# Performance work log

Measured on AMD Instinct MI355X. Metric: run time of the kernel, lower is better.

The kernel has to match this reference:

```python
import jax, jax.numpy as jnp
import numpy as np

N, E, D, G = 50000, 640000, 128, 64
STEPS = 4

def _leaky(z):
    return jnp.where(z >= 0, z, 0.01 * z)

def _lin(x, W, b):
    return x @ W.T + b

def setup_inputs() -> dict:
    key = jax.random.key(0)
    ks = jax.random.split(key, 16)
    s = 0.05
    inp = {
        "x": jax.random.normal(ks[0], (N, D), jnp.float32),
        "x_global": jax.random.normal(ks[1], (G, D), jnp.float32),
        "edge_attr": jax.random.normal(ks[2], (E, 2), jnp.float32),
        # per-step stacked parameters (torch Linear layout [out,in])
        "Wm": jax.random.normal(ks[3], (STEPS, D, D), jnp.float32) * s,
        "bm": jnp.zeros((STEPS, D), jnp.float32),
        "Wa": jax.random.normal(ks[4], (STEPS, D, 2 * D), jnp.float32) * s,
        "ba": jnp.zeros((STEPS, D), jnp.float32),
        "Wgate": jax.random.normal(ks[5], (STEPS, 1, D), jnp.float32) * s,
        "bgate": jnp.zeros((STEPS, 1), jnp.float32),
        "Wfeat": jax.random.normal(ks[6], (STEPS, D, D), jnp.float32) * s,
        "bfeat": jnp.zeros((STEPS, D), jnp.float32),
        "Wt": jax.random.normal(ks[7], (STEPS, D, 2 * D), jnp.float32) * s,
        "bt": jnp.zeros((STEPS, D), jnp.float32),
        "edge_index": jax.random.randint(ks[8], (2, E), 0, N, jnp.int32),
        "batch_ind": jnp.sort(jax.random.randint(ks[9], (N,), 0, G, jnp.int32)),
        "num_graphs": G,
    }
    return inp

def reference(x, x_global, edge_attr, Wm, bm, Wa, ba, Wgate, bgate, Wfeat, bfeat, Wt, bt, edge_index, batch_ind, num_graphs):
    src, dst = edge_index[0], edge_index[1]
    n = x.shape[0]
    for i in range(Wm.shape[0]):
        # GraphNet: gather -> Linear+LeakyReLU -> scatter-max -> concat -> Linear+LeakyReLU + residual
        msg = _leaky(_lin(x[src], Wm[i], bm[i]))                     # [E, agg]
        agg = jax.ops.segment_max(msg, dst, num_segments=n)
        agg = jnp.where(jnp.isfinite(agg), agg, 0.0)                 # PyG fills empty with 0
        x = _leaky(_lin(jnp.concatenate([x, agg], axis=1), Wa[i], ba[i])) + x
        # GlobalNode: attentional aggregation (segment softmax) + transform + residual
        gate = _lin(x, Wgate[i], bgate[i])[:, 0]                     # [N]
        feat = _leaky(_lin(x, Wfeat[i], bfeat[i]))                   # [N, D]
        gmax = jax.ops.segment_max(gate, batch_ind, num_segments=num_graphs)
        gmax = jnp.where(jnp.isfinite(gmax), gmax, 0.0)
        e = jnp.exp(gate - gmax[batch_ind])
        denom = jax.ops.segment_sum(e, batch_ind, num_segments=num_graphs)
        denom = jnp.where(denom == 0, 1.0, denom)
        alpha = e / denom[batch_ind]
        xg = jax.ops.segment_sum(alpha[:, None] * feat, batch_ind, num_segments=num_graphs)
        cat = jnp.concatenate([xg, x_global], axis=1)
        x_global = _leaky(_lin(cat, Wt[i], bt[i])) + x_global
    return (x, x_global)
```

## Files before the change

kernel.cpp:

```cpp
#include <hip/hip_runtime.h>
#include <hip/hip_bf16.h>

#define NN 50000
#define EE 640000
#define DD 128
#define GG 64
#define STEPS 4
#define XP 64
#define NB 196

static inline int cdiv(int a, int b) { return (a + b - 1) / b; }

typedef __attribute__((ext_vector_type(8))) short bf16x8;
typedef __attribute__((ext_vector_type(4))) float f32x4;

__device__ __forceinline__ float lk(float z) { return z >= 0.f ? z : 0.01f * z; }
__device__ __forceinline__ float b2f(short b) { return __uint_as_float(((unsigned)(unsigned short)b) << 16); }
__device__ __forceinline__ float b2fu(unsigned short b) { return __uint_as_float(((unsigned)b) << 16); }
__device__ __forceinline__ unsigned short f2b(float f) {
    unsigned u = __float_as_uint(f);
    return (unsigned short)((u + 0x7FFFu + ((u >> 16) & 1u)) >> 16);
}

__global__ void k_f2b(const float* __restrict__ in, unsigned short* __restrict__ out, int n4) {
    int i = blockIdx.x * blockDim.x + threadIdx.x;
    if (i < n4) {
        float4 v = reinterpret_cast<const float4*>(in)[i];
        ushort4 o;
        o.x = f2b(v.x); o.y = f2b(v.y); o.z = f2b(v.z); o.w = f2b(v.w);
        reinterpret_cast<ushort4*>(out)[i] = o;
    }
}

#define WC1 (STEPS * DD * DD / 4)
#define WC2 (STEPS * DD * 2 * DD / 4)
#define WC3 (STEPS * DD * DD / 4)
__global__ void k_wcvt(const float* __restrict__ Wm, const float* __restrict__ Wa, const float* __restrict__ Wf,
                       unsigned short* __restrict__ Wm_b, unsigned short* __restrict__ Wa_b,
                       unsigned short* __restrict__ Wf_b) {
    int i = blockIdx.x * blockDim.x + threadIdx.x;
    const float* src; unsigned short* dst; int j = i;
    if (j < WC1) { src = Wm; dst = Wm_b; }
    else {
        j -= WC1;
        if (j < WC2) { src = Wa; dst = Wa_b; }
        else {
            j -= WC2;
            if (j >= WC3) return;
            src = Wf; dst = Wf_b;
        }
    }
    float4 v = reinterpret_cast<const float4*>(src)[j];
    ushort4 o;
    o.x = f2b(v.x); o.y = f2b(v.y); o.z = f2b(v.z); o.w = f2b(v.w);
    reinterpret_cast<ushort4*>(dst)[j] = o;
}

__global__ void k_count(const int* __restrict__ dst, int* __restrict__ deg) {
    int e = blockIdx.x * blockDim.x + threadIdx.x;
    if (e < EE) atomicAdd(&deg[dst[e]], 1);
}

__global__ __launch_bounds__(256) void k_scan1(const int* __restrict__ deg, int* __restrict__ off,
                                               int* __restrict__ bsum) {
    __shared__ int ws[4];
    int tid = threadIdx.x, lane = tid & 63, wv = tid >> 6;
    int i = blockIdx.x * 256 + tid;
    int v = (i < NN) ? deg[i] : 0;
    int x = v;
    #pragma unroll
    for (int o = 1; o < 64; o <<= 1) { int t = __shfl_up(x, o); if (lane >= o) x += t; }
    if (lane == 63) ws[wv] = x;
    __syncthreads();
    int wbase = 0;
    #pragma unroll
    for (int p = 0; p < 3; ++p) if (p < wv) wbase += ws[p];
    if (i < NN) off[i] = wbase + x - v;
    if (tid == 255) bsum[blockIdx.x] = wbase + x;
}

__global__ __launch_bounds__(256) void k_scan2(const int* __restrict__ bsum, int* __restrict__ boff,
                                               int* __restrict__ off) {
    __shared__ int ws[4];
    int tid = threadIdx.x, lane = tid & 63, wv = tid >> 6;
    int v = (tid < NB) ? bsum[tid] : 0;
    int x = v;
    #pragma unroll
    for (int o = 1; o < 64; o <<= 1) { int t = __shfl_up(x, o); if (lane >= o) x += t; }
    if (lane == 63) ws[wv] = x;
    __syncthreads();
    int wbase = 0;
    #pragma unroll
    for (int p = 0; p < 3; ++p) if (p < wv) wbase += ws[p];
    if (tid < NB) boff[tid] = wbase + x - v;
    if (tid == 255) off[NN] = wbase + x;
}

__global__ __launch_bounds__(256) void k_scan3(const int* __restrict__ boff, int* __restrict__ off,
                                               int* __restrict__ cursor) {
    int i = blockIdx.x * 256 + threadIdx.x;
    if (i < NN) {
        int o = off[i] + boff[blockIdx.x];
        off[i] = o;
        cursor[i] = o;
    }
}

__global__ void k_fill(const int* __restrict__ src, const int* __restrict__ dst,
                       int* __restrict__ cursor, int* __restrict__ csr) {
    int e = blockIdx.x * blockDim.x + threadIdx.x;
    if (e < EE) {
        int d = dst[e];
        int p = atomicAdd(&cursor[d], 1);
        csr[p] = src[e];
    }
}

__global__ void k_goff(const int* __restrict__ batch, int* __restrict__ goff) {
    int i = blockIdx.x * blockDim.x + threadIdx.x;
    if (i >= NN) return;
    int b = batch[i];
    int prev = (i == 0) ? -1 : batch[i - 1];
    for (int g = prev + 1; g <= b; ++g) goff[g] = i;
    if (i == NN - 1) for (int g = b + 1; g <= GG; ++g) goff[g] = NN;
}

__global__ __launch_bounds__(256) void k_g128(
    const unsigned short* __restrict__ Xb, const unsigned short* __restrict__ W1,
    const float* __restrict__ b1, unsigned short* __restrict__ Yb1)
{
    __shared__ float sY[32 * 128];
    const int tid = threadIdx.x;
    const int wv = tid >> 6, lane = tid & 63;
    const int lo = lane & 15, hi = lane >> 4;
    const int rw = wv >> 1, cw = wv & 1;
    const int n0 = blockIdx.x * 32;
    const int arow = n0 + rw * 16 + lo;
    const bool rvalid = arow < NN;

    bf16x8 a[4];
    #pragma unroll
    for (int kc = 0; kc < 4; ++kc) {
        const int k = kc * 32 + hi * 8;
        a[kc] = rvalid ? *reinterpret_cast<const bf16x8*>(&Xb[(size_t)arow * 128 + k]) : (bf16x8)(short)0;
    }
    f32x4 acc[4];
    #pragma unroll
    for (int t = 0; t < 4; ++t) acc[t] = (f32x4){0.f,0.f,0.f,0.f};
    #pragma unroll
    for (int kc = 0; kc < 4; ++kc) {
        const int k = kc * 32 + hi * 8;
        #pragma unroll
        for (int t = 0; t < 4; ++t) {
            const int o = cw * 64 + t * 16 + lo;
            bf16x8 bv = *reinterpret_cast<const bf16x8*>(&W1[(size_t)o * 128 + k]);
            acc[t] = __builtin_amdgcn_mfma_f32_16x16x32_bf16(a[kc], bv, acc[t], 0, 0, 0);
        }
    }
    const int lrow = rw * 16 + hi * 4;
    const int swz = (hi & 1) << 4;
    #pragma unroll
    for (int t = 0; t < 4; ++t) {
        const int oc = cw * 64 + t * 16 + lo;
        const int col = oc ^ swz;
        const float bc = b1[oc];
        #pragma unroll
        for (int r = 0; r < 4; ++r) sY[(lrow + r) * 128 + col] = lk(acc[t][r] + bc);
    }
    __syncthreads();
    #pragma unroll
    for (int it = 0; it < 2; ++it) {
        const int idx = it * 256 + tid;
        const int row = idx >> 4, ub = (idx & 15) * 8;
        const int n = n0 + row;
        if (n < NN) {
            const int ubx = ub ^ (((row >> 2) & 1) << 4);
            bf16x8 ob;
            #pragma unroll
            for (int j = 0; j < 8; ++j) ob[j] = (short)f2b(sY[row * 128 + ubx + j]);
            *reinterpret_cast<bf16x8*>(&Yb1[(size_t)n * 128 + ub]) = ob;
        }
    }
}

template<bool MSG, bool LAST>
__global__ __launch_bounds__(256) void k_mega(
    const unsigned short* __restrict__ Xb, const unsigned short* __restrict__ Ab,
    const unsigned short* __restrict__ Wa, const float* __restrict__ ba,
    const float* __restrict__ wgf, const float* __restrict__ bgp,
    const unsigned short* __restrict__ Wf, const float* __restrict__ bfp,
    const unsigned short* __restrict__ Wm2, const float* __restrict__ bm2,
    float* __restrict__ Yf, unsigned short* __restrict__ Xbout,
    float* __restrict__ efac, unsigned short* __restrict__ featb,
    unsigned short* __restrict__ ybm)
{
    __shared__ float sY[32 * 128];
    __shared__ unsigned short sXn[32 * 136];
    const int tid = threadIdx.x;
    const int wv = tid >> 6, lane = tid & 63;
    const int lo = lane & 15, hi = lane >> 4;
    const int rw = wv >> 1, cw = wv & 1;
    const int n0 = blockIdx.x * 32;
    const int arow = n0 + rw * 16 + lo;
    const bool rvalid = arow < NN;

    bf16x8 a[8];
    #pragma unroll
    for (int kc = 0; kc < 8; ++kc) {
        const int k = kc * 32 + hi * 8;
        if (rvalid) {
            const unsigned short* base = (kc < 4) ? &Xb[(size_t)arow * 128 + k]
                                                  : &Ab[(size_t)arow * 128 + (k - 128)];
            a[kc] = *reinterpret_cast<const bf16x8*>(base);
        } else a[kc] = (bf16x8)(short)0;
    }

    f32x4 acc1[4];
    #pragma unroll
    for (int t = 0; t < 4; ++t) acc1[t] = (f32x4){0.f,0.f,0.f,0.f};
    #pragma unroll
    for (int kc = 0; kc < 8; ++kc) {
        const int k = kc * 32 + hi * 8;
        #pragma unroll
        for (int t = 0; t < 4; ++t) {
            const int o = cw * 64 + t * 16 + lo;
            bf16x8 bv = *reinterpret_cast<const bf16x8*>(&Wa[(size_t)o * 256 + k]);
            acc1[t] = __builtin_amdgcn_mfma_f32_16x16x32_bf16(a[kc], bv, acc1[t], 0, 0, 0);
        }
    }

    const int lrow = rw * 16 + hi * 4;
    const int swz = (hi & 1) << 4;
    #pragma unroll
    for (int t = 0; t < 4; ++t) {
        const int oc = cw * 64 + t * 16 + lo;
        const int col = oc ^ swz;
        const float bc = ba[oc];
        #pragma unroll
        for (int r = 0; r < 4; ++r) sY[(lrow + r) * 128 + col] = lk(acc1[t][r] + bc);
    }
    __syncthreads();

    {
        const float bg0 = bgp[0];
        #pragma unroll
        for (int it = 0; it < 4; ++it) {
            const int idx = it * 256 + tid;
            const int row = idx >> 5, u4 = (idx & 31) * 4;
            const int n = n0 + row;
            const bool valid = n < NN;
            const int ux = u4 ^ (((row >> 2) & 1) << 4);
            float4 v = *reinterpret_cast<const float4*>(&sY[row * 128 + ux]);
            if (valid) {
                ushort4 rb = *reinterpret_cast<const ushort4*>(&Xb[(size_t)n * 128 + u4]);
                v.x += b2fu(rb.x); v.y += b2fu(rb.y); v.z += b2fu(rb.z); v.w += b2fu(rb.w);
            }
            ushort4 ob;
            ob.x = f2b(v.x); ob.y = f2b(v.y); ob.z = f2b(v.z); ob.w = f2b(v.w);
            if (valid) {
                if (LAST) *reinterpret_cast<float4*>(&Yf[(size_t)n * 128 + u4]) = v;
                else      *reinterpret_cast<ushort4*>(&Xbout[(size_t)n * 128 + u4]) = ob;
            }
            *reinterpret_cast<ushort4*>(&sXn[row * 136 + u4]) = ob;
            float4 wg4 = *reinterpret_cast<const float4*>(&wgf[u4]);
            float gs = valid ? (v.x * wg4.x + v.y * wg4.y + v.z * wg4.z + v.w * wg4.w) : 0.f;
            #pragma unroll
            for (int sh = 16; sh > 0; sh >>= 1) gs += __shfl_xor(gs, sh);
            if ((lane & 31) == 0 && valid) efac[n] = __expf(gs + bg0);
        }
    }
    __syncthreads();

    bf16x8 a2[4];
    #pragma unroll
    for (int kc = 0; kc < 4; ++kc) {
        const int k = kc * 32 + hi * 8;
        a2[kc] = *reinterpret_cast<const bf16x8*>(&sXn[(rw * 16 + lo) * 136 + k]);
    }
    f32x4 accF[4], accM[4];
    #pragma unroll
    for (int t = 0; t < 4; ++t) { accF[t] = (f32x4){0.f,0.f,0.f,0.f}; accM[t] = (f32x4){0.f,0.f,0.f,0.f}; }
    #pragma unroll
    for (int kc = 0; kc < 4; ++kc) {
        const int k = kc * 32 + hi * 8;
        #pragma unroll
        for (int t = 0; t < 4; ++t) {
            const int o = cw * 64 + t * 16 + lo;
            bf16x8 bv = *reinterpret_cast<const bf16x8*>(&Wf[(size_t)o * 128 + k]);
            accF[t] = __builtin_amdgcn_mfma_f32_16x16x32_bf16(a2[kc], bv, accF[t], 0, 0, 0);
            if (MSG) {
                bf16x8 bv2 = *reinterpret_cast<const bf16x8*>(&Wm2[(size_t)o * 128 + k]);
                accM[t] = __builtin_amdgcn_mfma_f32_16x16x32_bf16(a2[kc], bv2, accM[t], 0, 0, 0);
            }
        }
    }
    __syncthreads();

    #pragma unroll
    for (int t = 0; t < 4; ++t) {
        const int oc = cw * 64 + t * 16 + lo;
        const int col = oc ^ swz;
        const float bc = bfp[oc];
        #pragma unroll
        for (int r = 0; r < 4; ++r) sY[(lrow + r) * 128 + col] = lk(accF[t][r] + bc);
    }
    __syncthreads();
    #pragma unroll
    for (int it = 0; it < 2; ++it) {
        const int idx = it * 256 + tid;
        const int row = idx >> 4, ub = (idx & 15) * 8;
        const int n = n0 + row;
        if (n < NN) {
            const int ubx = ub ^ (((row >> 2) & 1) << 4);
            bf16x8 ob;
            #pragma unroll
            for (int j = 0; j < 8; ++j) ob[j] = (short)f2b(sY[row * 128 + ubx + j]);
            *reinterpret_cast<bf16x8*>(&featb[(size_t)n * 128 + ub]) = ob;
        }
    }

    if (MSG) {
        __syncthreads();
        #pragma unroll
        for (int t = 0; t < 4; ++t) {
            const int oc = cw * 64 + t * 16 + lo;
            const int col = oc ^ swz;
            const float bc = bm2[oc];
            #pragma unroll
            for (int r = 0; r < 4; ++r) sY[(lrow + r) * 128 + col] = lk(accM[t][r] + bc);
        }
        __syncthreads();
        #pragma unroll
        for (int it = 0; it < 2; ++it) {
            const int idx = it * 256 + tid;
            const int row = idx >> 4, ub = (idx & 15) * 8;
            const int n = n0 + row;
            if (n < NN) {
                const int ubx = ub ^ (((row >> 2) & 1) << 4);
                bf16x8 ob;
                #pragma unroll
                for (int j = 0; j < 8; ++j) ob[j] = (short)f2b(sY[row * 128 + ubx + j]);
                *reinterpret_cast<bf16x8*>(&ybm[(size_t)n * 128 + ub]) = ob;
            }
        }
    }
}

__global__ __launch_bounds__(256) void k_aggmax(const unsigned short* __restrict__ yb,
                                                const int* __restrict__ off,
                                                const int* __restrict__ csr,
                                                unsigned short* __restrict__ aggb) {
    int gtid = blockIdx.x * blockDim.x + threadIdx.x;
    int node = gtid >> 6;
    if (node >= NN) return;
    int lane = threadIdx.x & 63;
    int slot = lane >> 4, c8 = (lane & 15) * 8;
    int b = off[node], e = off[node + 1];
    int deg = e - b;
    float m[8];
    #pragma unroll
    for (int j = 0; j < 8; ++j) m[j] = -3.4e38f;
    if (deg > 0) {
        int T = (deg + 7) >> 3;
        for (int it = 0; it < T; ++it) {
            int p0 = b + it * 8 + slot;
            int p1 = p0 + 4;
            int i0 = csr[p0 < e ? p0 : b];
            int i1 = csr[p1 < e ? p1 : b];
            bf16x8 v0 = *reinterpret_cast<const bf16x8*>(&yb[(size_t)i0 * 128 + c8]);
            bf16x8 v1 = *reinterpret_cast<const bf16x8*>(&yb[(size_t)i1 * 128 + c8]);
            #pragma unroll
            for (int j = 0; j < 8; ++j) m[j] = fmaxf(m[j], fmaxf(b2f(v0[j]), b2f(v1[j])));
        }
    }
    #pragma unroll
    for (int j = 0; j < 8; ++j) m[j] = fmaxf(m[j], __shfl_xor(m[j], 16));
    #pragma unroll
    for (int j = 0; j < 8; ++j) m[j] = fmaxf(m[j], __shfl_xor(m[j], 32));
    if (slot == 0) {
        bf16x8 o;
        #pragma unroll
        for (int j = 0; j < 8; ++j) o[j] = (deg > 0) ? (short)f2b(m[j]) : (short)0;
        *reinterpret_cast<bf16x8*>(&aggb[(size_t)node * 128 + c8]) = o;
    }
}

__global__ __launch_bounds__(128) void k_xgpart(const float* __restrict__ efac,
                                                const unsigned short* __restrict__ featb,
                                                const int* __restrict__ goff,
                                                float* __restrict__ part, float* __restrict__ parte) {
    int g = blockIdx.x >> 6, p = blockIdx.x & 63;
    int d = threadIdx.x;
    int b = goff[g], e = goff[g + 1];
    int len = e - b;
    int chunk = (len + XP - 1) / XP;
    int s0 = b + p * chunk;
    int s1 = min(e, s0 + chunk);
    float acc = 0.f, acce = 0.f;
    #pragma unroll 4
    for (int i = s0; i < s1; ++i) {
        float ev = efac[i];
        acce += ev;
        acc += ev * b2f(featb[(size_t)i * 128 + d]);
    }
    part[((size_t)g * XP + p) * 128 + d] = acc;
    if (d == 0) parte[(size_t)g * XP + p] = acce;
}

__global__ __launch_bounds__(128) void k_gtrans(const float* __restrict__ part, const float* __restrict__ parte,
                                                const float* __restrict__ Wt, const float* __restrict__ bt,
                                                float* __restrict__ xglob) {
    __shared__ float cat[256];
    int g = blockIdx.x;
    int o = threadIdx.x;
    float xgv = 0.f, se = 0.f;
    #pragma unroll
    for (int p = 0; p < XP; ++p) {
        xgv += part[((size_t)g * XP + p) * 128 + o];
        se  += parte[(size_t)g * XP + p];
    }
    if (se == 0.f) se = 1.f;
    cat[o] = xgv / se;
    cat[128 + o] = xglob[(size_t)g * 128 + o];
    __syncthreads();
    float accv = bt[o];
    const float4* w4 = reinterpret_cast<const float4*>(&Wt[(size_t)o * 256]);
    #pragma unroll 8
    for (int k4 = 0; k4 < 64; ++k4) {
        float4 wv = w4[k4];
        accv += cat[4 * k4 + 0] * wv.x + cat[4 * k4 + 1] * wv.y + cat[4 * k4 + 2] * wv.z + cat[4 * k4 + 3] * wv.w;
    }
    float outv = lk(accv) + cat[128 + o];
    xglob[(size_t)g * 128 + o] = outv;
}

extern "C" void kernel_launch(void* const* d_in, const int* in_sizes, int n_in,
                              void* d_out, int out_size, void* d_ws, size_t ws_size,
                              hipStream_t stream) {
    const float* x_in  = (const float*)d_in[0];
    const float* xg_in = (const float*)d_in[1];
    const float* Wm = (const float*)d_in[3];
    const float* bm = (const float*)d_in[4];
    const float* Wa = (const float*)d_in[5];
    const float* ba = (const float*)d_in[6];
    const float* Wg = (const float*)d_in[7];
    const float* bg = (const float*)d_in[8];
    const float* Wf = (const float*)d_in[9];
    const float* bf = (const float*)d_in[10];
    const float* Wt = (const float*)d_in[11];
    const float* bt = (const float*)d_in[12];
    const int* eidx  = (const int*)d_in[13];
    const int* batch = (const int*)d_in[14];

    float* xout  = (float*)d_out;
    float* xglob = xout + (size_t)NN * DD;

    char* w = (char*)d_ws;
    unsigned short* yb    = (unsigned short*)w; w += (size_t)NN * DD * 2;
    unsigned short* featb = (unsigned short*)w; w += (size_t)NN * DD * 2;
    unsigned short* aggb  = (unsigned short*)w; w += (size_t)NN * DD * 2;
    unsigned short* xb    = (unsigned short*)w; w += (size_t)NN * DD * 2;
    unsigned short* Wm_b  = (unsigned short*)w; w += (size_t)STEPS * DD * DD * 2;
    unsigned short* Wa_b  = (unsigned short*)w; w += (size_t)STEPS * DD * 2 * DD * 2;
    unsigned short* Wf_b  = (unsigned short*)w; w += (size_t)STEPS * DD * DD * 2;
    float* efac   = (float*)w; w += (size_t)NN * 4;
    float* part   = (float*)w; w += (size_t)GG * XP * DD * 4;
    float* parte  = (float*)w; w += (size_t)GG * XP * 4;
    int* deg    = (int*)w; w += (size_t)(NN + 1) * 4;
    int* off    = (int*)w; w += (size_t)(NN + 1) * 4;
    int* cursor = (int*)w; w += (size_t)NN * 4;
    int* csr    = (int*)w; w += (size_t)EE * 4;
    int* goff   = (int*)w; w += (size_t)(GG + 1) * 4;
    int* bsum   = (int*)w; w += (size_t)NB * 4;
    int* boff   = (int*)w; w += (size_t)NB * 4;

    const int* srcI = eidx;
    const int* dstI = eidx + EE;

    hipMemcpyAsync(xglob, xg_in, (size_t)GG * DD * 4, hipMemcpyDeviceToDevice, stream);

    k_f2b<<<cdiv(NN * DD / 4, 256), 256, 0, stream>>>(x_in, xb, NN * DD / 4);
    k_wcvt<<<cdiv(WC1 + WC2 + WC3, 256), 256, 0, stream>>>(Wm, Wa, Wf, Wm_b, Wa_b, Wf_b);

    hipMemsetAsync(deg, 0, (size_t)NN * 4, stream);
    k_count<<<cdiv(EE, 256), 256, 0, stream>>>(dstI, deg);
    k_scan1<<<NB, 256, 0, stream>>>(deg, off, bsum);
    k_scan2<<<1, 256, 0, stream>>>(bsum, boff, off);
    k_scan3<<<NB, 256, 0, stream>>>(boff, off, cursor);
    k_fill<<<cdiv(EE, 256), 256, 0, stream>>>(srcI, dstI, cursor, csr);
    k_goff<<<cdiv(NN, 256), 256, 0, stream>>>(batch, goff);

    const int gemmGrid = cdiv(NN, 32);
    const int aggGrid  = cdiv(NN * 64, 256);

    k_g128<<<gemmGrid, 256, 0, stream>>>(xb, Wm_b, bm, yb);

    for (int i = 0; i < STEPS; ++i) {
        const float* bai = ba + (size_t)i * DD;
        const unsigned short* Wai = Wa_b + (size_t)i * DD * 2 * DD;
        const float* Wgi = Wg + (size_t)i * DD;
        const float* bgi = bg + (size_t)i;
        const unsigned short* Wfi = Wf_b + (size_t)i * DD * DD;
        const float* bfi = bf + (size_t)i * DD;
        const float* Wti = Wt + (size_t)i * DD * 2 * DD;
        const float* bti = bt + (size_t)i * DD;

        k_aggmax<<<aggGrid, 256, 0, stream>>>(yb, off, csr, aggb);
        if (i < STEPS - 1) {
            const unsigned short* Wmn = Wm_b + (size_t)(i + 1) * DD * DD;
            const float* bmn = bm + (size_t)(i + 1) * DD;
            k_mega<true, false><<<gemmGrid, 256, 0, stream>>>(
                xb, aggb, Wai, bai, Wgi, bgi, Wfi, bfi, Wmn, bmn,
                nullptr, xb, efac, featb, yb);
        } else {
            k_mega<false, true><<<gemmGrid, 256, 0, stream>>>(
                xb, aggb, Wai, bai, Wgi, bgi, Wfi, bfi, nullptr, nullptr,
                xout, nullptr, efac, featb, nullptr);
        }
        k_xgpart<<<GG * XP, 128, 0, stream>>>(efac, featb, goff, part, parte);
        k_gtrans<<<GG, 128, 0, stream>>>(part, parte, Wti, bti, xglob);
    }
}
```

Measured before the change: 517.7 us.

## Fuse CSR gather scatter-max into the GNN GEMM kernel with ping-pong message buffers

Measured after the change: 539.7 us. 4.3% more time.

```diff
diff --git a/kernel.cpp b/kernel.cpp
--- a/kernel.cpp
+++ b/kernel.cpp
@@ -185,7 +185,8 @@
 
 template<bool MSG, bool LAST>
 __global__ __launch_bounds__(256) void k_mega(
-    const unsigned short* __restrict__ Xb, const unsigned short* __restrict__ Ab,
+    const unsigned short* __restrict__ Xb, const unsigned short* __restrict__ yb_in,
+    const int* __restrict__ off, const int* __restrict__ csr,
     const unsigned short* __restrict__ Wa, const float* __restrict__ ba,
     const float* __restrict__ wgf, const float* __restrict__ bgp,
     const unsigned short* __restrict__ Wf, const float* __restrict__ bfp,
@@ -194,8 +195,8 @@
     float* __restrict__ efac, unsigned short* __restrict__ featb,
     unsigned short* __restrict__ ybm)
 {
-    __shared__ float sY[32 * 128];
-    __shared__ unsigned short sXn[32 * 136];
+    __shared__ unsigned short bufA[32 * 136];
+    __shared__ unsigned short bufB[32 * 136];
     const int tid = threadIdx.x;
     const int wv = tid >> 6, lane = tid & 63;
     const int lo = lane & 15, hi = lane >> 4;
@@ -206,14 +207,56 @@
 
     bf16x8 a[8];
     #pragma unroll
-    for (int kc = 0; kc < 8; ++kc) {
+    for (int kc = 0; kc < 4; ++kc) {
         const int k = kc * 32 + hi * 8;
-        if (rvalid) {
-            const unsigned short* base = (kc < 4) ? &Xb[(size_t)arow * 128 + k]
-                                                  : &Ab[(size_t)arow * 128 + (k - 128)];
-            a[kc] = *reinterpret_cast<const bf16x8*>(base);
-        } else a[kc] = (bf16x8)(short)0;
-    }
+        a[kc] = rvalid ? *reinterpret_cast<const bf16x8*>(&Xb[(size_t)arow * 128 + k]) : (bf16x8)(short)0;
+    }
+
+    const int c8 = lo * 8;
+    for (int nn = 0; nn < 8; ++nn) {
+        const int lr = wv * 8 + nn;
+        const int node = n0 + lr;
+        if (node < NN) {
+            int b = off[node], e = off[node + 1];
+            int deg = e - b;
+            float m[8];
+            #pragma unroll
+            for (int j = 0; j < 8; ++j) m[j] = -3.4e38f;
+            if (deg > 0) {
+                int T = (deg + 7) >> 3;
+                for (int it = 0; it < T; ++it) {
+                    int p0 = b + it * 8 + hi;
+                    int p1 = p0 + 4;
+                    int i0 = csr[p0 < e ? p0 : b];
+                    int i1 = csr[p1 < e ? p1 : b];
+                    bf16x8 v0 = *reinterpret_cast<const bf16x8*>(&yb_in[(size_t)i0 * 128 + c8]);
+                    bf16x8 v1 = *reinterpret_cast<const bf16x8*>(&yb_in[(size_t)i1 * 128 + c8]);
+                    #pragma unroll
+                    for (int j = 0; j < 8; ++j) m[j] = fmaxf(m[j], fmaxf(b2f(v0[j]), b2f(v1[j])));
+                }
+            }
+            #pragma unroll
+            for (int j = 0; j < 8; ++j) m[j] = fmaxf(m[j], __shfl_xor(m[j], 16));
+            #pragma unroll
+            for (int j = 0; j < 8; ++j) m[j] = fmaxf(m[j], __shfl_xor(m[j], 32));
+            if (hi == 0) {
+                bf16x8 o;
+                #pragma unroll
+                for (int j = 0; j < 8; ++j) o[j] = (deg > 0) ? (short)f2b(m[j]) : (short)0;
+                *reinterpret_cast<bf16x8*>(&bufA[lr * 136 + c8]) = o;
+            }
+        } else if (hi == 0) {
+            *reinterpret_cast<bf16x8*>(&bufA[lr * 136 + c8]) = (bf16x8)(short)0;
+        }
+    }
+    __syncthreads();
+
+    #pragma unroll
+    for (int kc = 4; kc < 8; ++kc) {
+        const int k = (kc - 4) * 32 + hi * 8;
+        a[kc] = *reinterpret_cast<const bf16x8*>(&bufA[(rw * 16 + lo) * 136 + k]);
+    }
+    __syncthreads();
 
     f32x4 acc1[4];
     #pragma unroll
@@ -237,7 +280,7 @@
         const int col = oc ^ swz;
         const float bc = ba[oc];
         #pragma unroll
-        for (int r = 0; r < 4; ++r) sY[(lrow + r) * 128 + col] = lk(acc1[t][r] + bc);
+        for (int r = 0; r < 4; ++r) bufA[(lrow + r) * 136 + col] = f2b(lk(acc1[t][r] + bc));
     }
     __syncthreads();
 
@@ -250,7 +293,9 @@
             const int n = n0 + row;
             const bool valid = n < NN;
             const int ux = u4 ^ (((row >> 2) & 1) << 4);
-            float4 v = *reinterpret_cast<const float4*>(&sY[row * 128 + ux]);
+            ushort4 sv = *reinterpret_cast<const ushort4*>(&bufA[row * 136 + ux]);
+            float4 v;
+            v.x = b2fu(sv.x); v.y = b2fu(sv.y); v.z = b2fu(sv.z); v.w = b2fu(sv.w);
             if (valid) {
                 ushort4 rb = *reinterpret_cast<const ushort4*>(&Xb[(size_t)n * 128 + u4]);
                 v.x += b2fu(rb.x); v.y += b2fu(rb.y); v.z += b2fu(rb.z); v.w += b2fu(rb.w);
@@ -261,7 +306,7 @@
                 if (LAST) *reinterpret_cast<float4*>(&Yf[(size_t)n * 128 + u4]) = v;
                 else      *reinterpret_cast<ushort4*>(&Xbout[(size_t)n * 128 + u4]) = ob;
             }
-            *reinterpret_cast<ushort4*>(&sXn[row * 136 + u4]) = ob;
+            *reinterpret_cast<ushort4*>(&bufB[row * 136 + u4]) = ob;
             float4 wg4 = *reinterpret_cast<const float4*>(&wgf[u4]);
             float gs = valid ? (v.x * wg4.x + v.y * wg4.y + v.z * wg4.z + v.w * wg4.w) : 0.f;
             #pragma unroll
@@ -275,8 +320,10 @@
     #pragma unroll
     for (int kc = 0; kc < 4; ++kc) {
         const int k = kc * 32 + hi * 8;
-        a2[kc] = *reinterpret_cast<const bf16x8*>(&sXn[(rw * 16 + lo) * 136 + k]);
-    }
+        a2[kc] = *reinterpret_cast<const bf16x8*>(&bufB[(rw * 16 + lo) * 136 + k]);
+    }
+    __syncthreads();
+
     f32x4 accF[4], accM[4];
     #pragma unroll
     for (int t = 0; t < 4; ++t) { accF[t] = (f32x4){0.f,0.f,0.f,0.f}; accM[t] = (f32x4){0.f,0.f,0.f,0.f}; }
@@ -294,17 +341,22 @@
             }
         }
     }
-    __syncthreads();
 
     #pragma unroll
     for (int t = 0; t < 4; ++t) {
         const int oc = cw * 64 + t * 16 + lo;
         const int col = oc ^ swz;
-        const float bc = bfp[oc];
-        #pragma unroll
-        for (int r = 0; r < 4; ++r) sY[(lrow + r) * 128 + col] = lk(accF[t][r] + bc);
-    }
-    __syncthreads();
+        const float bcF = bfp[oc];
+        #pragma unroll
+        for (int r = 0; r < 4; ++r) bufB[(lrow + r) * 136 + col] = f2b(lk(accF[t][r] + bcF));
+        if (MSG) {
+            const float bcM = bm2[oc];
+            #pragma unroll
+            for (int r = 0; r < 4; ++r) bufA[(lrow + r) * 136 + col] = f2b(lk(accM[t][r] + bcM));
+        }
+    }
+    __syncthreads();
+
     #pragma unroll
     for (int it = 0; it < 2; ++it) {
         const int idx = it * 256 + tid;
@@ -312,76 +364,12 @@
         const int n = n0 + row;
         if (n < NN) {
             const int ubx = ub ^ (((row >> 2) & 1) << 4);
-            bf16x8 ob;
-            #pragma unroll
-            for (int j = 0; j < 8; ++j) ob[j] = (short)f2b(sY[row * 128 + ubx + j]);
-            *reinterpret_cast<bf16x8*>(&featb[(size_t)n * 128 + ub]) = ob;
-        }
-    }
-
-    if (MSG) {
-        __syncthreads();
-        #pragma unroll
-        for (int t = 0; t < 4; ++t) {
-            const int oc = cw * 64 + t * 16 + lo;
-            const int col = oc ^ swz;
-            const float bc = bm2[oc];
-            #pragma unroll
-            for (int r = 0; r < 4; ++r) sY[(lrow + r) * 128 + col] = lk(accM[t][r] + bc);
-        }
-        __syncthreads();
-        #pragma unroll
-        for (int it = 0; it < 2; ++it) {
-            const int idx = it * 256 + tid;
-            const int row = idx >> 4, ub = (idx & 15) * 8;
-            const int n = n0 + row;
-            if (n < NN) {
-                const int ubx = ub ^ (((row >> 2) & 1) << 4);
-                bf16x8 ob;
-                #pragma unroll
-                for (int j = 0; j < 8; ++j) ob[j] = (short)f2b(sY[row * 128 + ubx + j]);
-                *reinterpret_cast<bf16x8*>(&ybm[(size_t)n * 128 + ub]) = ob;
-            }
-        }
-    }
-}
-
-__global__ __launch_bounds__(256) void k_aggmax(const unsigned short* __restrict__ yb,
-                                                const int* __restrict__ off,
-                                                const int* __restrict__ csr,
-                                                unsigned short* __restrict__ aggb) {
-    int gtid = blockIdx.x * blockDim.x + threadIdx.x;
-    int node = gtid >> 6;
-    if (node >= NN) return;
-    int lane = threadIdx.x & 63;
-    int slot = lane >> 4, c8 = (lane & 15) * 8;
-    int b = off[node], e = off[node + 1];
-    int deg = e - b;
-    float m[8];
-    #pragma unroll
-    for (int j = 0; j < 8; ++j) m[j] = -3.4e38f;
-    if (deg > 0) {
-        int T = (deg + 7) >> 3;
-        for (int it = 0; it < T; ++it) {
-            int p0 = b + it * 8 + slot;
-            int p1 = p0 + 4;
-            int i0 = csr[p0 < e ? p0 : b];
-            int i1 = csr[p1 < e ? p1 : b];
-            bf16x8 v0 = *reinterpret_cast<const bf16x8*>(&yb[(size_t)i0 * 128 + c8]);
-            bf16x8 v1 = *reinterpret_cast<const bf16x8*>(&yb[(size_t)i1 * 128 + c8]);
-            #pragma unroll
-            for (int j = 0; j < 8; ++j) m[j] = fmaxf(m[j], fmaxf(b2f(v0[j]), b2f(v1[j])));
-        }
-    }
-    #pragma unroll
-    for (int j = 0; j < 8; ++j) m[j] = fmaxf(m[j], __shfl_xor(m[j], 16));
-    #pragma unroll
-    for (int j = 0; j < 8; ++j) m[j] = fmaxf(m[j], __shfl_xor(m[j], 32));
-    if (slot == 0) {
-        bf16x8 o;
-        #pragma unroll
-        for (int j = 0; j < 8; ++j) o[j] = (deg > 0) ? (short)f2b(m[j]) : (short)0;
-        *reinterpret_cast<bf16x8*>(&aggb[(size_t)node * 128 + c8]) = o;
+            *reinterpret_cast<bf16x8*>(&featb[(size_t)n * 128 + ub]) =
+                *reinterpret_cast<const bf16x8*>(&bufB[row * 136 + ubx]);
+            if (MSG)
+                *reinterpret_cast<bf16x8*>(&ybm[(size_t)n * 128 + ub]) =
+                    *reinterpret_cast<const bf16x8*>(&bufA[row * 136 + ubx]);
+        }
     }
 }
 
@@ -456,9 +444,9 @@
     float* xglob = xout + (size_t)NN * DD;
 
     char* w = (char*)d_ws;
-    unsigned short* yb    = (unsigned short*)w; w += (size_t)NN * DD * 2;
+    unsigned short* yb0   = (unsigned short*)w; w += (size_t)NN * DD * 2;
+    unsigned short* yb1   = (unsigned short*)w; w += (size_t)NN * DD * 2;
     unsigned short* featb = (unsigned short*)w; w += (size_t)NN * DD * 2;
-    unsigned short* aggb  = (unsigned short*)w; w += (size_t)NN * DD * 2;
     unsigned short* xb    = (unsigned short*)w; w += (size_t)NN * DD * 2;
     unsigned short* Wm_b  = (unsigned short*)w; w += (size_t)STEPS * DD * DD * 2;
     unsigned short* Wa_b  = (unsigned short*)w; w += (size_t)STEPS * DD * 2 * DD * 2;
@@ -474,6 +462,8 @@
     int* bsum   = (int*)w; w += (size_t)NB * 4;
     int* boff   = (int*)w; w += (size_t)NB * 4;
 
+    unsigned short* ybuf[2] = { yb0, yb1 };
+
     const int* srcI = eidx;
     const int* dstI = eidx + EE;
 
@@ -491,9 +481,8 @@
     k_goff<<<cdiv(NN, 256), 256, 0, stream>>>(batch, goff);
 
     const int gemmGrid = cdiv(NN, 32);
-    const int aggGrid  = cdiv(NN * 64, 256);
-
-    k_g128<<<gemmGrid, 256, 0, stream>>>(xb, Wm_b, bm, yb);
+
+    k_g128<<<gemmGrid, 256, 0, stream>>>(xb, Wm_b, bm, ybuf[0]);
 
     for (int i = 0; i < STEPS; ++i) {
         const float* bai = ba + (size_t)i * DD;
@@ -504,17 +493,18 @@
         const float* bfi = bf + (size_t)i * DD;
         const float* Wti = Wt + (size_t)i * DD * 2 * DD;
         const float* bti = bt + (size_t)i * DD;
-
-        k_aggmax<<<aggGrid, 256, 0, stream>>>(yb, off, csr, aggb);
+        const unsigned short* ybIn  = ybuf[i & 1];
+        unsigned short* ybOut = ybuf[(i + 1) & 1];
+
         if (i < STEPS - 1) {
             const unsigned short* Wmn = Wm_b + (size_t)(i + 1) * DD * DD;
             const float* bmn = bm + (size_t)(i + 1) * DD;
             k_mega<true, false><<<gemmGrid, 256, 0, stream>>>(
-                xb, aggb, Wai, bai, Wgi, bgi, Wfi, bfi, Wmn, bmn,
-                nullptr, xb, efac, featb, yb);
+                xb, ybIn, off, csr, Wai, bai, Wgi, bgi, Wfi, bfi, Wmn, bmn,
+                nullptr, xb, efac, featb, ybOut);
         } else {
             k_mega<false, true><<<gemmGrid, 256, 0, stream>>>(
-                xb, aggb, Wai, bai, Wgi, bgi, Wfi, bfi, nullptr, nullptr,
+                xb, ybIn, off, csr, Wai, bai, Wgi, bgi, Wfi, bfi, nullptr, nullptr,
                 xout, nullptr, efac, featb, nullptr);
         }
         k_xgpart<<<GG * XP, 128, 0, stream>>>(efac, featb, goff, part, parte);
```
